# Optimization experiments

Hardware: AMD Instinct MI355X
Metric: run time of the kernel (lower is better)

## Reference

```python
import jax, jax.numpy as jnp
import numpy as np

B, N, H = 128, 1024, 128          # graphs, nodes per graph, hidden size
K1, K2, K3 = 512, 256, 128        # ceil(ratio^l * N), ratio = 0.5
DEG = 8                           # avg degree
E = B * N * DEG                   # total edges (fixed, masked after pooling)


def gcn_conv(x, row, col, mask, W, b, n):
    h = x @ W
    deg = jax.ops.segment_sum(mask, col, num_segments=n) + 1.0  # + self loop
    dinv = jax.lax.rsqrt(deg)
    coef = (dinv[row] * dinv[col] * mask)[:, None]
    agg = jax.ops.segment_sum(h[row] * coef, col, num_segments=n)
    return agg + h * (dinv * dinv)[:, None] + b  # self-loop term + bias


def topk_pool(x, row, col, mask, p, n_graphs, n_per, k):
    # PyG TopKPooling: y = x.p/||p||, keep per-graph top-k, x' = x[perm]*tanh(y[perm])
    score = (x @ p) / jnp.linalg.norm(p)
    vals, idx = jax.lax.top_k(score.reshape(n_graphs, n_per), k)  # [B, k]
    sel = (idx + (jnp.arange(n_graphs) * n_per)[:, None]).reshape(-1)
    xs = x[sel] * jnp.tanh(vals.reshape(-1))[:, None]
    # relabel edges; drop edges touching removed nodes via mask
    newid = jnp.full((n_graphs * n_per,), -1, jnp.int32).at[sel].set(
        jnp.arange(n_graphs * k, dtype=jnp.int32))
    nr, nc = newid[row], newid[col]
    nmask = mask * ((nr >= 0) & (nc >= 0)).astype(mask.dtype)
    return xs, jnp.maximum(nr, 0), jnp.maximum(nc, 0), nmask


def readout(x, n_graphs, k):
    # cat([gmp, gap]) with contiguous equal-size graphs
    xg = x.reshape(n_graphs, k, -1)
    return jnp.concatenate([xg.max(axis=1), xg.mean(axis=1)], axis=1)


def _forward(x, edge_row, edge_col, W1, b1, p1, W2, b2, p2, W3, b3, p3):
    mask = jnp.ones((E,), x.dtype)
    h = jax.nn.relu(gcn_conv(x, edge_row, edge_col, mask, W1, b1, B * N))
    x1, r, c, m = topk_pool(h, edge_row, edge_col, mask, p1, B, N, K1)
    out = readout(x1, B, K1)
    h = jax.nn.relu(gcn_conv(x1, r, c, m, W2, b2, B * K1))
    x2, r, c, m = topk_pool(h, r, c, m, p2, B, K1, K2)
    out = out + readout(x2, B, K2)
    h = jax.nn.relu(gcn_conv(x2, r, c, m, W3, b3, B * K2))
    x3, r, c, m = topk_pool(h, r, c, m, p3, B, K2, K3)
    out = out + readout(x3, B, K3)
    return out  # [B, 2*H]


def setup_inputs() -> dict:
    key = jax.random.key(0)
    ks = jax.random.split(key, 12)
    x = jax.random.normal(ks[0], (B * N, H), jnp.float32)
    off = (jnp.arange(B, dtype=jnp.int32) * N)[:, None]
    edge_row = (jax.random.randint(ks[1], (B, N * DEG), 0, N, jnp.int32) + off).reshape(-1)
    edge_col = (jax.random.randint(ks[2], (B, N * DEG), 0, N, jnp.int32) + off).reshape(-1)
    s = 1.0 / np.sqrt(H)
    params = {}
    for i, tag in enumerate(["1", "2", "3"]):
        params["W" + tag] = jax.random.normal(ks[3 + 3 * i], (H, H), jnp.float32) * s
        params["b" + tag] = jnp.zeros((H,), jnp.float32)
        params["p" + tag] = jax.random.normal(ks[4 + 3 * i], (H,), jnp.float32)
    return {"x": x, "edge_row": edge_row, "edge_col": edge_col, **params}


def reference(x, edge_row, edge_col, W1, b1, p1, W2, b2, p2, W3, b3, p3):
    return _forward(x, edge_row, edge_col, W1, b1, p1, W2, b2, p2, W3, b3, p3)
```

## Files before the change

kernel.cpp:

```cpp
#include <hip/hip_runtime.h>
#include <math.h>

#define BG   128
#define NPER 1024
#define HDIM 128
#define NEDGE (BG * NPER * 8)
#define NMAX (BG * NPER)
#define EPG  (NEDGE / BG)
#define CAP  48
#define PRE  16

typedef __attribute__((ext_vector_type(8))) short s16x8;
typedef __attribute__((ext_vector_type(4))) float f32x4;

static __device__ __forceinline__ ushort f2bf(float f) {
  uint u = __float_as_uint(f);
  return (ushort)((u + 0x7fffu + ((u >> 16) & 1u)) >> 16);
}
static __device__ __forceinline__ float bf2f(ushort h) {
  return __uint_as_float(((uint)h) << 16);
}

extern __shared__ float ldsbuf[];


__global__ __launch_bounds__(1024) void countfill_lds_kernel(
    const int* __restrict__ cr, const int* __restrict__ cc,
    int* __restrict__ cnt, int* __restrict__ meta8,
    int* __restrict__ srcext, int* __restrict__ order,
    int* __restrict__ odeg) {
  int* smeta = (int*)ldsbuf;
  int* scnt  = smeta + NPER * PRE;
  int* sbb   = scnt + NPER;
  int g = blockIdx.x, t = threadIdx.x;
  scnt[t] = 0;
  if (t < 2) sbb[t] = 0;
  __syncthreads();

  const int4* cr4 = (const int4*)(cr + (size_t)g * EPG);
  const int4* cc4 = (const int4*)(cc + (size_t)g * EPG);
  #pragma unroll
  for (int i = 0; i < 2; ++i) {
    int4 r = cr4[t * 2 + i];
    int4 c = cc4[t * 2 + i];
    int rl, cl, pos;
    cl = c.x & (NPER - 1); rl = r.x & (NPER - 1);
    pos = atomicAdd(&scnt[cl], 1);
    if (pos < PRE) smeta[cl * PRE + pos] = rl;
    else if (pos < CAP) srcext[((size_t)g * NPER + cl) * CAP + pos] = rl;
    cl = c.y & (NPER - 1); rl = r.y & (NPER - 1);
    pos = atomicAdd(&scnt[cl], 1);
    if (pos < PRE) smeta[cl * PRE + pos] = rl;
    else if (pos < CAP) srcext[((size_t)g * NPER + cl) * CAP + pos] = rl;
    cl = c.z & (NPER - 1); rl = r.z & (NPER - 1);
    pos = atomicAdd(&scnt[cl], 1);
    if (pos < PRE) smeta[cl * PRE + pos] = rl;
    else if (pos < CAP) srcext[((size_t)g * NPER + cl) * CAP + pos] = rl;
    cl = c.w & (NPER - 1); rl = r.w & (NPER - 1);
    pos = atomicAdd(&scnt[cl], 1);
    if (pos < PRE) smeta[cl * PRE + pos] = rl;
    else if (pos < CAP) srcext[((size_t)g * NPER + cl) * CAP + pos] = rl;
  }
  __syncthreads();

  int4* mo = (int4*)(meta8 + (size_t)g * NPER * PRE);
  const int4* sm4 = (const int4*)smeta;
  #pragma unroll
  for (int i = 0; i < 4; ++i) mo[i * 1024 + t] = sm4[i * 1024 + t];
  int d = scnt[t];
  cnt[g * NPER + t] = d;

  int bkt = d > 8 ? 1 : 0;
  int bpos = atomicAdd(&sbb[bkt], 1);
  __syncthreads();
  int slot = bkt ? sbb[0] + bpos : bpos;
  order[g * NPER + slot] = t;
  odeg[g * NPER + slot] = d;
}


__global__ __launch_bounds__(1024) void agg_lds_kernel(
    const float* __restrict__ x, float* __restrict__ z,
    const int* __restrict__ meta8, const int* __restrict__ srcext,
    const int* __restrict__ deg, const int* __restrict__ order,
    const int* __restrict__ odeg, int npg) {
  float* sX = ldsbuf;
  float* sDinv = sX + npg * 32;
  int g = blockIdx.x >> 2;
  int chunk = blockIdx.x & 3;
  int t = threadIdx.x;
  int base = g * npg;

  const float4* x4 = (const float4*)x;
  float4* sX4 = (float4*)sX;
  for (int i = t; i < npg * 8; i += 1024) {
    int r = i >> 3, l8 = i & 7;
    float dv = rsqrtf((float)deg[base + r] + 1.0f);
    float4 v = x4[(size_t)(base + r) * 32 + chunk * 8 + l8];
    v.x *= dv; v.y *= dv; v.z *= dv; v.w *= dv;
    sX4[i] = v;
  }
  for (int i = t; i < npg; i += 1024)
    sDinv[i] = rsqrtf((float)deg[base + i] + 1.0f);

  int dl = t >> 3, l = t & 7;
  const int4* m4 = (const int4*)meta8;
  float4* z4 = (float4*)z;

  int ordc = order[base + dl];
  int dpc  = odeg[base + dl];
  int ordn = order[base + dl + 128];
  int dpn  = odeg[base + dl + 128];
  int4 c0 = m4[(size_t)(base + ordc) * 4 + 0];
  int4 c1 = m4[(size_t)(base + ordc) * 4 + 1];
  int4 c2 = {0, 0, 0, 0}, c3 = {0, 0, 0, 0};
  if (dpc > 8) {
    c2 = m4[(size_t)(base + ordc) * 4 + 2];
    c3 = m4[(size_t)(base + ordc) * 4 + 3];
  }

  __syncthreads();

  for (int slot = dl; slot < npg; slot += 128) {
    int ordn2 = ordn, dpn2 = dpn;
    if (slot + 256 < npg) {
      ordn2 = order[base + slot + 256];
      dpn2  = odeg[base + slot + 256];
    }
    int4 n0 = {0,0,0,0}, n1 = {0,0,0,0}, n2 = {0,0,0,0}, n3 = {0,0,0,0};
    if (slot + 128 < npg) {
      n0 = m4[(size_t)(base + ordn) * 4 + 0];
      n1 = m4[(size_t)(base + ordn) * 4 + 1];
      if (dpn > 8) {
        n2 = m4[(size_t)(base + ordn) * 4 + 2];
        n3 = m4[(size_t)(base + ordn) * 4 + 3];
      }
    }

    int dst = ordc;
    int node = base + dst;
    int d = dpc > CAP ? CAP : dpc;
    int dp = d > PRE ? PRE : d;
    float dc = sDinv[dst];

    int sA0 = (0 < dp) ? c0.x : dst;
    int sA1 = (1 < dp) ? c0.y : dst;
    int sA2 = (2 < dp) ? c0.z : dst;
    int sA3 = (3 < dp) ? c0.w : dst;
    int sA4 = (4 < dp) ? c1.x : dst;
    int sA5 = (5 < dp) ? c1.y : dst;
    int sA6 = (6 < dp) ? c1.z : dst;
    int sA7 = (7 < dp) ? c1.w : dst;
    float4 w  = sX4[dst * 8 + l];
    float4 p0 = sX4[sA0 * 8 + l];
    float4 p1 = sX4[sA1 * 8 + l];
    float4 p2 = sX4[sA2 * 8 + l];
    float4 p3 = sX4[sA3 * 8 + l];
    float4 p4 = sX4[sA4 * 8 + l];
    float4 p5 = sX4[sA5 * 8 + l];
    float4 p6 = sX4[sA6 * 8 + l];
    float4 p7 = sX4[sA7 * 8 + l];
    float4 a0, a1, a2, a3;
    a0.x = w.x + p0.x; a0.y = w.y + p0.y; a0.z = w.z + p0.z; a0.w = w.w + p0.w;
    a1.x = p1.x + p5.x; a1.y = p1.y + p5.y; a1.z = p1.z + p5.z; a1.w = p1.w + p5.w;
    a2.x = p2.x + p6.x; a2.y = p2.y + p6.y; a2.z = p2.z + p6.z; a2.w = p2.w + p6.w;
    a3.x = p3.x + p7.x; a3.y = p3.y + p7.y; a3.z = p3.z + p7.z; a3.w = p3.w + p7.w;
    a0.x += p4.x; a0.y += p4.y; a0.z += p4.z; a0.w += p4.w;

    int nslots = 8;
    if (dp > 8) {
      int sB0 = (8 < dp)  ? c2.x : dst;
      int sB1 = (9 < dp)  ? c2.y : dst;
      int sB2 = (10 < dp) ? c2.z : dst;
      int sB3 = (11 < dp) ? c2.w : dst;
      int sB4 = (12 < dp) ? c3.x : dst;
      int sB5 = (13 < dp) ? c3.y : dst;
      int sB6 = (14 < dp) ? c3.z : dst;
      int sB7 = (15 < dp) ? c3.w : dst;
      float4 q0 = sX4[sB0 * 8 + l];
      float4 q1 = sX4[sB1 * 8 + l];
      float4 q2 = sX4[sB2 * 8 + l];
      float4 q3 = sX4[sB3 * 8 + l];
      float4 q4 = sX4[sB4 * 8 + l];
      float4 q5 = sX4[sB5 * 8 + l];
      float4 q6 = sX4[sB6 * 8 + l];
      float4 q7 = sX4[sB7 * 8 + l];
      a0.x += q0.x; a0.y += q0.y; a0.z += q0.z; a0.w += q0.w;
      a1.x += q1.x; a1.y += q1.y; a1.z += q1.z; a1.w += q1.w;
      a2.x += q2.x; a2.y += q2.y; a2.z += q2.z; a2.w += q2.w;
      a3.x += q3.x; a3.y += q3.y; a3.z += q3.z; a3.w += q3.w;
      a0.x += q4.x; a0.y += q4.y; a0.z += q4.z; a0.w += q4.w;
      a1.x += q5.x; a1.y += q5.y; a1.z += q5.z; a1.w += q5.w;
      a2.x += q6.x; a2.y += q6.y; a2.z += q6.z; a2.w += q6.w;
      a3.x += q7.x; a3.y += q7.y; a3.z += q7.z; a3.w += q7.w;
      nslots = 16;
    }

    if (d > PRE) {
      for (int e2 = PRE; e2 < d; ++e2) {
        int rl = srcext[(size_t)node * CAP + e2];
        float4 v0 = sX4[rl * 8 + l];
        a0.x += v0.x; a0.y += v0.y; a0.z += v0.z; a0.w += v0.w;
      }
    }

    float corr = (float)(nslots - dp);
    float4 o;
    o.x = (a0.x + a1.x + a2.x + a3.x - corr * w.x) * dc;
    o.y = (a0.y + a1.y + a2.y + a3.y - corr * w.y) * dc;
    o.z = (a0.z + a1.z + a2.z + a3.z - corr * w.z) * dc;
    o.w = (a0.w + a1.w + a2.w + a3.w - corr * w.w) * dc;
    z4[(size_t)node * 32 + chunk * 8 + l] = o;

    ordc = ordn; dpc = dpn; ordn = ordn2; dpn = dpn2;
    c0 = n0; c1 = n1; c2 = n2; c3 = n3;
  }
}


__global__ __launch_bounds__(256) void wsplit_kernel(
    const float* __restrict__ W0, const float* __restrict__ W1,
    const float* __restrict__ W2, ushort* __restrict__ wpk) {
  int id = blockIdx.x * 256 + threadIdx.x;
  int L = id >> 14;
  int r = id & 16383;
  int i = r & 7;
  int lane = (r >> 3) & 63;
  int nt = (r >> 9) & 7;
  int kt = (r >> 12) & 3;
  int k = kt * 32 + (lane >> 4) * 8 + i;
  int n = nt * 16 + (lane & 15);
  const float* W = (L == 0) ? W0 : (L == 1) ? W1 : W2;
  float v = W[k * HDIM + n];
  ushort h = f2bf(v);
  float r1 = v - bf2f(h);
  ushort m = f2bf(r1);
  ushort lo = f2bf(r1 - bf2f(m));
  size_t base = (size_t)L * 3 * 16384 + (size_t)r;
  wpk[base] = h;
  wpk[base + 16384] = m;
  wpk[base + 32768] = lo;
}


__global__ __launch_bounds__(256) void conv_mfma_kernel(
    float* __restrict__ zh, const ushort* __restrict__ wpk,
    const float* __restrict__ bias, const float* __restrict__ p,
    float* __restrict__ score) {
  __shared__ short sB[2][12288];
  int t = threadIdx.x;
  int wv = t >> 6, l = t & 63;
  int lr = l & 15, lq = l >> 4;
  int arowA = blockIdx.x * 128 + wv * 16 + lr;
  int arowB = arowA + 64;
  const float* zrowA = zh + (size_t)arowA * HDIM + lq * 8;
  const float* zrowB = zh + (size_t)arowB * HDIM + lq * 8;

  const int4* wp4 = (const int4*)wpk;
  int i0 = t, i1 = t + 256, i2 = t + 512;
  int i3 = t + 768, i4 = t + 1024, i5 = t + 1280;
  int s0 = (i0 >> 9) * 2048 + (i0 & 511);
  int s1 = (i1 >> 9) * 2048 + (i1 & 511);
  int s2 = (i2 >> 9) * 2048 + (i2 & 511);
  int s3 = (i3 >> 9) * 2048 + (i3 & 511);
  int s4 = (i4 >> 9) * 2048 + (i4 & 511);
  int s5 = (i5 >> 9) * 2048 + (i5 & 511);

  int4 rg0 = wp4[s0], rg1 = wp4[s1], rg2 = wp4[s2];
  int4 rg3 = wp4[s3], rg4 = wp4[s4], rg5 = wp4[s5];
  float4 cA0 = ((const float4*)zrowA)[0];
  float4 cA1 = ((const float4*)zrowA)[1];
  float4 cB0 = ((const float4*)zrowB)[0];
  float4 cB1 = ((const float4*)zrowB)[1];
  {
    int4* sw = (int4*)sB[0];
    sw[i0] = rg0; sw[i1] = rg1; sw[i2] = rg2;
    sw[i3] = rg3; sw[i4] = rg4; sw[i5] = rg5;
  }
  __syncthreads();

  f32x4 accA[8], accB[8];
  #pragma unroll
  for (int nt = 0; nt < 8; ++nt) { accA[nt] = (f32x4)(0.f); accB[nt] = (f32x4)(0.f); }

  for (int kt = 0; kt < 4; ++kt) {
    int cur = kt & 1;
    float4 nA0, nA1, nB0, nB1;
    if (kt < 3) {
      int kb = (kt + 1) * 512;
      rg0 = wp4[s0 + kb]; rg1 = wp4[s1 + kb]; rg2 = wp4[s2 + kb];
      rg3 = wp4[s3 + kb]; rg4 = wp4[s4 + kb]; rg5 = wp4[s5 + kb];
      nA0 = ((const float4*)(zrowA + (kt + 1) * 32))[0];
      nA1 = ((const float4*)(zrowA + (kt + 1) * 32))[1];
      nB0 = ((const float4*)(zrowB + (kt + 1) * 32))[0];
      nB1 = ((const float4*)(zrowB + (kt + 1) * 32))[1];
    }

    s16x8 ahA, amA, alA, ahB, amB, alB;
    float fA[8] = {cA0.x, cA0.y, cA0.z, cA0.w, cA1.x, cA1.y, cA1.z, cA1.w};
    float fB[8] = {cB0.x, cB0.y, cB0.z, cB0.w, cB1.x, cB1.y, cB1.z, cB1.w};
    #pragma unroll
    for (int i = 0; i < 8; ++i) {
      ushort h = f2bf(fA[i]);
      float r1 = fA[i] - bf2f(h);
      ushort m = f2bf(r1);
      ushort lo = f2bf(r1 - bf2f(m));
      ahA[i] = (short)h; amA[i] = (short)m; alA[i] = (short)lo;
      h = f2bf(fB[i]);
      r1 = fB[i] - bf2f(h);
      m = f2bf(r1);
      lo = f2bf(r1 - bf2f(m));
      ahB[i] = (short)h; amB[i] = (short)m; alB[i] = (short)lo;
    }

    const s16x8* sb = (const s16x8*)sB[cur];
    #pragma unroll
    for (int nt = 0; nt < 8; ++nt) {
      s16x8 bh = sb[nt * 64 + l];
      s16x8 bm = sb[512 + nt * 64 + l];
      s16x8 bl = sb[1024 + nt * 64 + l];
      accA[nt] = __builtin_amdgcn_mfma_f32_16x16x32_bf16(ahA, bh, accA[nt], 0, 0, 0);
      accA[nt] = __builtin_amdgcn_mfma_f32_16x16x32_bf16(ahA, bm, accA[nt], 0, 0, 0);
      accA[nt] = __builtin_amdgcn_mfma_f32_16x16x32_bf16(amA, bh, accA[nt], 0, 0, 0);
      accA[nt] = __builtin_amdgcn_mfma_f32_16x16x32_bf16(ahA, bl, accA[nt], 0, 0, 0);
      accA[nt] = __builtin_amdgcn_mfma_f32_16x16x32_bf16(alA, bh, accA[nt], 0, 0, 0);
      accA[nt] = __builtin_amdgcn_mfma_f32_16x16x32_bf16(amA, bm, accA[nt], 0, 0, 0);
      accB[nt] = __builtin_amdgcn_mfma_f32_16x16x32_bf16(ahB, bh, accB[nt], 0, 0, 0);
      accB[nt] = __builtin_amdgcn_mfma_f32_16x16x32_bf16(ahB, bm, accB[nt], 0, 0, 0);
      accB[nt] = __builtin_amdgcn_mfma_f32_16x16x32_bf16(amB, bh, accB[nt], 0, 0, 0);
      accB[nt] = __builtin_amdgcn_mfma_f32_16x16x32_bf16(ahB, bl, accB[nt], 0, 0, 0);
      accB[nt] = __builtin_amdgcn_mfma_f32_16x16x32_bf16(alB, bh, accB[nt], 0, 0, 0);
      accB[nt] = __builtin_amdgcn_mfma_f32_16x16x32_bf16(amB, bm, accB[nt], 0, 0, 0);
    }
    __syncthreads();
    if (kt < 3) {
      int4* sw = (int4*)sB[cur ^ 1];
      sw[i0] = rg0; sw[i1] = rg1; sw[i2] = rg2;
      sw[i3] = rg3; sw[i4] = rg4; sw[i5] = rg5;
      cA0 = nA0; cA1 = nA1; cB0 = nB0; cB1 = nB1;
    }
    __syncthreads();
  }

  int orowA = blockIdx.x * 128 + wv * 16 + lq * 4;
  int orowB = orowA + 64;
  float partA[4] = {0.f, 0.f, 0.f, 0.f};
  float partB[4] = {0.f, 0.f, 0.f, 0.f};
  #pragma unroll
  for (int nt = 0; nt < 8; ++nt) {
    float bv = bias[nt * 16 + lr];
    float pv = p[nt * 16 + lr];
    #pragma unroll
    for (int j = 0; j < 4; ++j) {
      float hA = fmaxf(accA[nt][j] + bv, 0.f);
      partA[j] += hA * pv;
      zh[(size_t)(orowA + j) * HDIM + nt * 16 + lr] = hA;
      float hB = fmaxf(accB[nt][j] + bv, 0.f);
      partB[j] += hB * pv;
      zh[(size_t)(orowB + j) * HDIM + nt * 16 + lr] = hB;
    }
  }
  #pragma unroll
  for (int j = 0; j < 4; ++j) {
    #pragma unroll
    for (int s = 1; s < 16; s <<= 1) {
      partA[j] += __shfl_xor(partA[j], s);
      partB[j] += __shfl_xor(partB[j], s);
    }
    if (lr == 0) {
      score[orowA + j] = partA[j];
      score[orowB + j] = partB[j];
    }
  }
}


__global__ __launch_bounds__(1024) void topk_mega_kernel(
    const float* __restrict__ score, const float* __restrict__ p,
    const float* __restrict__ h, float* __restrict__ xo,
    const int* __restrict__ in_r, const int* __restrict__ in_c,
    int* __restrict__ out_r, int* __restrict__ out_c,
    int* __restrict__ meta8, int* __restrict__ srcext,
    int* __restrict__ cnt, float* __restrict__ acc,
    int* __restrict__ order, int* __restrict__ odeg,
    float* __restrict__ outf, int P, int K, int L) {
  __shared__ float sv[1024];
  __shared__ int si[1024];
  __shared__ int snew[1024];
  __shared__ int scnt[512];
  __shared__ int bb[2];
  __shared__ float s_pn;
  __shared__ float4 smx[32][32], ssm[32][32];
  int g = blockIdx.x;
  int t = threadIdx.x;

  if (L < 2 && t < 512) scnt[t] = 0;
  if (t < 2) bb[t] = 0;
  snew[t] = -1;
  if (t < 128) { float v = p[t]; sv[t] = v * v; }
  __syncthreads();
  for (int off = 64; off; off >>= 1) {
    if (t < off) sv[t] += sv[t + off];
    __syncthreads();
  }
  if (t == 0) s_pn = sqrtf(sv[0]);
  __syncthreads();
  float pn = s_pn;

  sv[t] = score[(size_t)g * P + t];
  si[t] = t;
  for (int size = 2; size <= P; size <<= 1) {
    for (int stride = size >> 1; stride; stride >>= 1) {
      __syncthreads();
      int j = t ^ stride;
      if (j > t) {
        float a = sv[t], b = sv[j];
        int ia = si[t], ib = si[j];
        bool tFirst = (a > b) || (a == b && ia < ib);
        bool up = ((t & size) == 0);
        if (up ? !tFirst : tFirst) {
          sv[t] = b; sv[j] = a;
          si[t] = ib; si[j] = ia;
        }
      }
    }
  }
  __syncthreads();
  if (t < K) {
    snew[si[t]] = t;
    sv[t] = tanhf(sv[t] / pn);
  }
  __syncthreads();

  int lane = t & 31, grp = t >> 5;
  const float4* h4 = (const float4*)h;
  float4* xo4 = (float4*)xo;
  size_t hbase = (size_t)g * P * 32;
  float4 mx = make_float4(-INFINITY, -INFINITY, -INFINITY, -INFINITY);
  float4 sm = make_float4(0.f, 0.f, 0.f, 0.f);
  #pragma unroll
  for (int i = 0; i < 16; ++i) {
    int j = grp * 16 + i;
    float th = sv[j];
    float4 v = h4[hbase + (size_t)si[j] * 32 + lane];
    v.x *= th; v.y *= th; v.z *= th; v.w *= th;
    xo4[((size_t)g * K + j) * 32 + lane] = v;
    mx.x = fmaxf(mx.x, v.x); mx.y = fmaxf(mx.y, v.y);
    mx.z = fmaxf(mx.z, v.z); mx.w = fmaxf(mx.w, v.w);
    sm.x += v.x; sm.y += v.y; sm.z += v.z; sm.w += v.w;
  }
  smx[grp][lane] = mx;
  ssm[grp][lane] = sm;
  __syncthreads();
  int ngrp = P >> 5;
  if (grp == 0) {
    for (int s2 = 1; s2 < ngrp; ++s2) {
      float4 m2 = smx[s2][lane], s3 = ssm[s2][lane];
      mx.x = fmaxf(mx.x, m2.x); mx.y = fmaxf(mx.y, m2.y);
      mx.z = fmaxf(mx.z, m2.z); mx.w = fmaxf(mx.w, m2.w);
      sm.x += s3.x; sm.y += s3.y; sm.z += s3.z; sm.w += s3.w;
    }
    int c0 = lane * 4;
    if (L < 2) {
      float* amax = acc + (size_t)L * BG * 256 + (size_t)g * 256;
      float* asum = amax + 128;
      amax[c0 + 0] = mx.x; amax[c0 + 1] = mx.y;
      amax[c0 + 2] = mx.z; amax[c0 + 3] = mx.w;
      asum[c0 + 0] = sm.x; asum[c0 + 1] = sm.y;
      asum[c0 + 2] = sm.z; asum[c0 + 3] = sm.w;
    } else {
      sv[c0 + 0] = mx.x; sv[c0 + 1] = mx.y;
      sv[c0 + 2] = mx.z; sv[c0 + 3] = mx.w;
      sv[128 + c0 + 0] = sm.x; sv[128 + c0 + 1] = sm.y;
      sv[128 + c0 + 2] = sm.z; sv[128 + c0 + 3] = sm.w;
    }
  }

  if (L == 2) {
    __syncthreads();
    float v;
    const float* a0 = acc + (size_t)g * 256;
    const float* a1 = acc + (size_t)BG * 256 + (size_t)g * 256;
    if (t < 128) {
      v = a0[t] + a1[t] + sv[t];
    } else {
      v = a0[t] * (1.f / 512.f) + a1[t] * (1.f / 256.f) + sv[t] * (1.f / 128.f);
    }
    outf[g * 256 + t] = v;
    return;
  }

  int ept = EPG / P;
  int ebase = g * EPG;
  for (int i = 0; i < ept; ++i) {
    int e = ebase + i * P + t;
    int r = in_r[e];
    int nr = -1, nc = -1;
    if (r >= 0) {
      nr = snew[r & (P - 1)];
      nc = snew[in_c[e] & (P - 1)];
    }
    bool ok = (nr >= 0) && (nc >= 0);
    out_r[e] = ok ? g * K + nr : -1;
    out_c[e] = ok ? g * K + nc : -1;
    if (ok) {
      int pos = atomicAdd(&scnt[nc], 1);
      size_t gnode = (size_t)g * K + nc;
      if (pos < PRE) {
        meta8[gnode * PRE + pos] = nr;
      } else if (pos < CAP) {
        srcext[gnode * CAP + pos] = nr;
      }
    }
  }
  __syncthreads();
  if (t < K) cnt[g * K + t] = scnt[t];

  int bkt = 0, bpos = 0, bdeg = 0;
  if (t < K) {
    bdeg = scnt[t];
    bkt = bdeg > 8 ? 1 : 0;
    bpos = atomicAdd(&bb[bkt], 1);
  }
  __syncthreads();
  if (t < K) {
    int slot = bkt ? bb[0] + bpos : bpos;
    order[g * K + slot] = t;
    odeg[g * K + slot] = bdeg;
  }
}


extern "C" void kernel_launch(void* const* d_in, const int* in_sizes, int n_in,
                              void* d_out, int out_size, void* d_ws, size_t ws_size,
                              hipStream_t stream) {
  const float* x0 = (const float*)d_in[0];
  const int* erow = (const int*)d_in[1];
  const int* ecol = (const int*)d_in[2];
  const float* Wm[3] = {(const float*)d_in[3], (const float*)d_in[6], (const float*)d_in[9]};
  const float* bm[3] = {(const float*)d_in[4], (const float*)d_in[7], (const float*)d_in[10]};
  const float* pm[3] = {(const float*)d_in[5], (const float*)d_in[8], (const float*)d_in[11]};

  char* w = (char*)d_ws;
  size_t off = 0;
  auto alloc = [&](size_t bytes) -> void* {
    void* ptr = w + off;
    off = (off + bytes + 255) & ~(size_t)255;
    return ptr;
  };
  int* cur_row = (int*)alloc((size_t)NEDGE * 4);
  int* cur_col = (int*)alloc((size_t)NEDGE * 4);
  int* meta8   = (int*)alloc((size_t)NMAX * PRE * 4);
  int* srcext  = (int*)alloc((size_t)NMAX * CAP * 4);
  int* cnt     = (int*)alloc((size_t)NMAX * 4);
  int* order   = (int*)alloc((size_t)NMAX * 4);
  int* odeg    = (int*)alloc((size_t)NMAX * 4);
  float* score = (float*)alloc((size_t)NMAX * 4);
  float* acc   = (float*)alloc((size_t)2 * BG * 256 * 4);
  float* zh    = (float*)alloc((size_t)NMAX * HDIM * 4);
  float* x1    = (float*)alloc((size_t)BG * 512 * HDIM * 4);
  float* x2    = (float*)alloc((size_t)BG * 256 * HDIM * 4);
  float* x3    = (float*)alloc((size_t)BG * 128 * HDIM * 4);
  ushort* wpk  = (ushort*)alloc((size_t)3 * 3 * 16384 * 2);

  hipFuncSetAttribute((const void*)agg_lds_kernel,
                      hipFuncAttributeMaxDynamicSharedMemorySize, 152 * 1024);
  hipFuncSetAttribute((const void*)countfill_lds_kernel,
                      hipFuncAttributeMaxDynamicSharedMemorySize, 72 * 1024);

  size_t cfLds = (size_t)(NPER * PRE + NPER + 2) * 4;
  countfill_lds_kernel<<<BG, 1024, cfLds, stream>>>(
      erow, ecol, cnt, meta8, srcext, order, odeg);
  wsplit_kernel<<<(3 * 16384) / 256, 256, 0, stream>>>(Wm[0], Wm[1], Wm[2], wpk);

  const float* xin = x0;
  float* xout[3] = {x1, x2, x3};
  int Ps[3] = {1024, 512, 256};

  for (int L = 0; L < 3; ++L) {
    int P = Ps[L];
    int K = P >> 1;
    int n = BG * P;
    const int* in_r = (L == 0) ? erow : cur_row;
    const int* in_c = (L == 0) ? ecol : cur_col;
    size_t ldsBytes = (size_t)(P * 33) * 4;

    agg_lds_kernel<<<BG * 4, 1024, ldsBytes, stream>>>(
        xin, zh, meta8, srcext, cnt, order, odeg, P);
    conv_mfma_kernel<<<n / 128, 256, 0, stream>>>(
        zh, wpk + (size_t)L * 3 * 16384, bm[L], pm[L], score);
    topk_mega_kernel<<<BG, P, 0, stream>>>(
        score, pm[L], zh, xout[L], in_r, in_c, cur_row, cur_col,
        meta8, srcext, cnt, acc, order, odeg, (float*)d_out, P, K, L);
    xin = xout[L];
  }
}
```

Baseline: 317.6 us.

## Pack neighbor lists as 16-bit indices and transpose LDS feature layout

Stores the first 16 neighbor source indices per node as ushort rather than int, halving the meta array and its global loads and LDS footprint in countfill. The agg kernel's LDS feature tile is also transposed to a lane-major layout with a padded stride (npg+2), which is meant to change the LDS bank-conflict pattern of the gathered float4 reads. This adds unpacking shifts and masks per neighbor, and relies on local node ids fitting in 16 bits.

Result: no change. 316.1 us (-0.5%).

```diff
diff --git a/kernel.cpp b/kernel.cpp
--- a/kernel.cpp
+++ b/kernel.cpp
@@ -26,11 +26,11 @@
 
 __global__ __launch_bounds__(1024) void countfill_lds_kernel(
     const int* __restrict__ cr, const int* __restrict__ cc,
-    int* __restrict__ cnt, int* __restrict__ meta8,
+    int* __restrict__ cnt, ushort* __restrict__ meta16,
     int* __restrict__ srcext, int* __restrict__ order,
     int* __restrict__ odeg) {
-  int* smeta = (int*)ldsbuf;
-  int* scnt  = smeta + NPER * PRE;
+  ushort* smeta = (ushort*)ldsbuf;
+  int* scnt  = (int*)(smeta + NPER * PRE);
   int* sbb   = scnt + NPER;
   int g = blockIdx.x, t = threadIdx.x;
   scnt[t] = 0;
@@ -46,27 +46,27 @@
     int rl, cl, pos;
     cl = c.x & (NPER - 1); rl = r.x & (NPER - 1);
     pos = atomicAdd(&scnt[cl], 1);
-    if (pos < PRE) smeta[cl * PRE + pos] = rl;
+    if (pos < PRE) smeta[cl * PRE + pos] = (ushort)rl;
     else if (pos < CAP) srcext[((size_t)g * NPER + cl) * CAP + pos] = rl;
     cl = c.y & (NPER - 1); rl = r.y & (NPER - 1);
     pos = atomicAdd(&scnt[cl], 1);
-    if (pos < PRE) smeta[cl * PRE + pos] = rl;
+    if (pos < PRE) smeta[cl * PRE + pos] = (ushort)rl;
     else if (pos < CAP) srcext[((size_t)g * NPER + cl) * CAP + pos] = rl;
     cl = c.z & (NPER - 1); rl = r.z & (NPER - 1);
     pos = atomicAdd(&scnt[cl], 1);
-    if (pos < PRE) smeta[cl * PRE + pos] = rl;
+    if (pos < PRE) smeta[cl * PRE + pos] = (ushort)rl;
     else if (pos < CAP) srcext[((size_t)g * NPER + cl) * CAP + pos] = rl;
     cl = c.w & (NPER - 1); rl = r.w & (NPER - 1);
     pos = atomicAdd(&scnt[cl], 1);
-    if (pos < PRE) smeta[cl * PRE + pos] = rl;
+    if (pos < PRE) smeta[cl * PRE + pos] = (ushort)rl;
     else if (pos < CAP) srcext[((size_t)g * NPER + cl) * CAP + pos] = rl;
   }
   __syncthreads();
 
-  int4* mo = (int4*)(meta8 + (size_t)g * NPER * PRE);
+  int4* mo = (int4*)(meta16 + (size_t)g * NPER * PRE);
   const int4* sm4 = (const int4*)smeta;
   #pragma unroll
-  for (int i = 0; i < 4; ++i) mo[i * 1024 + t] = sm4[i * 1024 + t];
+  for (int i = 0; i < 2; ++i) mo[i * 1024 + t] = sm4[i * 1024 + t];
   int d = scnt[t];
   cnt[g * NPER + t] = d;
 
@@ -81,43 +81,39 @@
 
 __global__ __launch_bounds__(1024) void agg_lds_kernel(
     const float* __restrict__ x, float* __restrict__ z,
-    const int* __restrict__ meta8, const int* __restrict__ srcext,
+    const ushort* __restrict__ meta16, const int* __restrict__ srcext,
     const int* __restrict__ deg, const int* __restrict__ order,
     const int* __restrict__ odeg, int npg) {
-  float* sX = ldsbuf;
-  float* sDinv = sX + npg * 32;
+  const int PSTR = npg + 2;
+  float4* sX4 = (float4*)ldsbuf;
+  float* sDinv = ldsbuf + 8 * PSTR * 4;
   int g = blockIdx.x >> 2;
   int chunk = blockIdx.x & 3;
   int t = threadIdx.x;
   int base = g * npg;
 
   const float4* x4 = (const float4*)x;
-  float4* sX4 = (float4*)sX;
   for (int i = t; i < npg * 8; i += 1024) {
     int r = i >> 3, l8 = i & 7;
     float dv = rsqrtf((float)deg[base + r] + 1.0f);
     float4 v = x4[(size_t)(base + r) * 32 + chunk * 8 + l8];
     v.x *= dv; v.y *= dv; v.z *= dv; v.w *= dv;
-    sX4[i] = v;
+    sX4[l8 * PSTR + r] = v;
   }
   for (int i = t; i < npg; i += 1024)
     sDinv[i] = rsqrtf((float)deg[base + i] + 1.0f);
 
   int dl = t >> 3, l = t & 7;
-  const int4* m4 = (const int4*)meta8;
+  const int4* m4 = (const int4*)meta16;
   float4* z4 = (float4*)z;
 
   int ordc = order[base + dl];
   int dpc  = odeg[base + dl];
   int ordn = order[base + dl + 128];
   int dpn  = odeg[base + dl + 128];
-  int4 c0 = m4[(size_t)(base + ordc) * 4 + 0];
-  int4 c1 = m4[(size_t)(base + ordc) * 4 + 1];
-  int4 c2 = {0, 0, 0, 0}, c3 = {0, 0, 0, 0};
-  if (dpc > 8) {
-    c2 = m4[(size_t)(base + ordc) * 4 + 2];
-    c3 = m4[(size_t)(base + ordc) * 4 + 3];
-  }
+  int4 c0 = m4[(size_t)(base + ordc) * 2 + 0];
+  int4 c1 = {0, 0, 0, 0};
+  if (dpc > 8) c1 = m4[(size_t)(base + ordc) * 2 + 1];
 
   __syncthreads();
 
@@ -127,14 +123,10 @@
       ordn2 = order[base + slot + 256];
       dpn2  = odeg[base + slot + 256];
     }
-    int4 n0 = {0,0,0,0}, n1 = {0,0,0,0}, n2 = {0,0,0,0}, n3 = {0,0,0,0};
+    int4 n0 = {0,0,0,0}, n1 = {0,0,0,0};
     if (slot + 128 < npg) {
-      n0 = m4[(size_t)(base + ordn) * 4 + 0];
-      n1 = m4[(size_t)(base + ordn) * 4 + 1];
-      if (dpn > 8) {
-        n2 = m4[(size_t)(base + ordn) * 4 + 2];
-        n3 = m4[(size_t)(base + ordn) * 4 + 3];
-      }
+      n0 = m4[(size_t)(base + ordn) * 2 + 0];
+      if (dpn > 8) n1 = m4[(size_t)(base + ordn) * 2 + 1];
     }
 
     int dst = ordc;
@@ -143,23 +135,29 @@
     int dp = d > PRE ? PRE : d;
     float dc = sDinv[dst];
 
-    int sA0 = (0 < dp) ? c0.x : dst;
-    int sA1 = (1 < dp) ? c0.y : dst;
-    int sA2 = (2 < dp) ? c0.z : dst;
-    int sA3 = (3 < dp) ? c0.w : dst;
-    int sA4 = (4 < dp) ? c1.x : dst;
-    int sA5 = (5 < dp) ? c1.y : dst;
-    int sA6 = (6 < dp) ? c1.z : dst;
-    int sA7 = (7 < dp) ? c1.w : dst;
-    float4 w  = sX4[dst * 8 + l];
-    float4 p0 = sX4[sA0 * 8 + l];
-    float4 p1 = sX4[sA1 * 8 + l];
-    float4 p2 = sX4[sA2 * 8 + l];
-    float4 p3 = sX4[sA3 * 8 + l];
-    float4 p4 = sX4[sA4 * 8 + l];
-    float4 p5 = sX4[sA5 * 8 + l];
-    float4 p6 = sX4[sA6 * 8 + l];
-    float4 p7 = sX4[sA7 * 8 + l];
+    int e0 = c0.x & 0xffff, e1 = ((uint)c0.x) >> 16;
+    int e2 = c0.y & 0xffff, e3 = ((uint)c0.y) >> 16;
+    int e4 = c0.z & 0xffff, e5 = ((uint)c0.z) >> 16;
+    int e6 = c0.w & 0xffff, e7 = ((uint)c0.w) >> 16;
+
+    int sA0 = (0 < dp) ? e0 : dst;
+    int sA1 = (1 < dp) ? e1 : dst;
+    int sA2 = (2 < dp) ? e2 : dst;
+    int sA3 = (3 < dp) ? e3 : dst;
+    int sA4 = (4 < dp) ? e4 : dst;
+    int sA5 = (5 < dp) ? e5 : dst;
+    int sA6 = (6 < dp) ? e6 : dst;
+    int sA7 = (7 < dp) ? e7 : dst;
+    int pb = l * PSTR;
+    float4 w  = sX4[pb + dst];
+    float4 p0 = sX4[pb + sA0];
+    float4 p1 = sX4[pb + sA1];
+    float4 p2 = sX4[pb + sA2];
+    float4 p3 = sX4[pb + sA3];
+    float4 p4 = sX4[pb + sA4];
+    float4 p5 = sX4[pb + sA5];
+    float4 p6 = sX4[pb + sA6];
+    float4 p7 = sX4[pb + sA7];
     float4 a0, a1, a2, a3;
     a0.x = w.x + p0.x; a0.y = w.y + p0.y; a0.z = w.z + p0.z; a0.w = w.w + p0.w;
     a1.x = p1.x + p5.x; a1.y = p1.y + p5.y; a1.z = p1.z + p5.z; a1.w = p1.w + p5.w;
@@ -169,22 +167,26 @@
 
     int nslots = 8;
     if (dp > 8) {
-      int sB0 = (8 < dp)  ? c2.x : dst;
-      int sB1 = (9 < dp)  ? c2.y : dst;
-      int sB2 = (10 < dp) ? c2.z : dst;
-      int sB3 = (11 < dp) ? c2.w : dst;
-      int sB4 = (12 < dp) ? c3.x : dst;
-      int sB5 = (13 < dp) ? c3.y : dst;
-      int sB6 = (14 < dp) ? c3.z : dst;
-      int sB7 = (15 < dp) ? c3.w : dst;
-      float4 q0 = sX4[sB0 * 8 + l];
-      float4 q1 = sX4[sB1 * 8 + l];
-      float4 q2 = sX4[sB2 * 8 + l];
-      float4 q3 = sX4[sB3 * 8 + l];
-      float4 q4 = sX4[sB4 * 8 + l];
-      float4 q5 = sX4[sB5 * 8 + l];
-      float4 q6 = sX4[sB6 * 8 + l];
-      float4 q7 = sX4[sB7 * 8 + l];
+      int f0 = c1.x & 0xffff, f1 = ((uint)c1.x) >> 16;
+      int f2 = c1.y & 0xffff, f3 = ((uint)c1.y) >> 16;
+      int f4 = c1.z & 0xffff, f5 = ((uint)c1.z) >> 16;
+      int f6 = c1.w & 0xffff, f7 = ((uint)c1.w) >> 16;
+      int sB0 = (8 < dp)  ? f0 : dst;
+      int sB1 = (9 < dp)  ? f1 : dst;
+      int sB2 = (10 < dp) ? f2 : dst;
+      int sB3 = (11 < dp) ? f3 : dst;
+      int sB4 = (12 < dp) ? f4 : dst;
+      int sB5 = (13 < dp) ? f5 : dst;
+      int sB6 = (14 < dp) ? f6 : dst;
+      int sB7 = (15 < dp) ? f7 : dst;
+      float4 q0 = sX4[pb + sB0];
+      float4 q1 = sX4[pb + sB1];
+      float4 q2 = sX4[pb + sB2];
+      float4 q3 = sX4[pb + sB3];
+      float4 q4 = sX4[pb + sB4];
+      float4 q5 = sX4[pb + sB5];
+      float4 q6 = sX4[pb + sB6];
+      float4 q7 = sX4[pb + sB7];
       a0.x += q0.x; a0.y += q0.y; a0.z += q0.z; a0.w += q0.w;
       a1.x += q1.x; a1.y += q1.y; a1.z += q1.z; a1.w += q1.w;
       a2.x += q2.x; a2.y += q2.y; a2.z += q2.z; a2.w += q2.w;
@@ -197,9 +199,9 @@
     }
 
     if (d > PRE) {
-      for (int e2 = PRE; e2 < d; ++e2) {
-        int rl = srcext[(size_t)node * CAP + e2];
-        float4 v0 = sX4[rl * 8 + l];
+      for (int e2i = PRE; e2i < d; ++e2i) {
+        int rl = srcext[(size_t)node * CAP + e2i];
+        float4 v0 = sX4[pb + rl];
         a0.x += v0.x; a0.y += v0.y; a0.z += v0.z; a0.w += v0.w;
       }
     }
@@ -213,7 +215,7 @@
     z4[(size_t)node * 32 + chunk * 8 + l] = o;
 
     ordc = ordn; dpc = dpn; ordn = ordn2; dpn = dpn2;
-    c0 = n0; c1 = n1; c2 = n2; c3 = n3;
+    c0 = n0; c1 = n1;
   }
 }
 
@@ -380,7 +382,7 @@
     const float* __restrict__ h, float* __restrict__ xo,
     const int* __restrict__ in_r, const int* __restrict__ in_c,
     int* __restrict__ out_r, int* __restrict__ out_c,
-    int* __restrict__ meta8, int* __restrict__ srcext,
+    ushort* __restrict__ meta16, int* __restrict__ srcext,
     int* __restrict__ cnt, float* __restrict__ acc,
     int* __restrict__ order, int* __restrict__ odeg,
     float* __restrict__ outf, int P, int K, int L) {
@@ -507,7 +509,7 @@
       int pos = atomicAdd(&scnt[nc], 1);
       size_t gnode = (size_t)g * K + nc;
       if (pos < PRE) {
-        meta8[gnode * PRE + pos] = nr;
+        meta16[gnode * PRE + pos] = (ushort)nr;
       } else if (pos < CAP) {
         srcext[gnode * CAP + pos] = nr;
       }
@@ -550,7 +552,7 @@
   };
   int* cur_row = (int*)alloc((size_t)NEDGE * 4);
   int* cur_col = (int*)alloc((size_t)NEDGE * 4);
-  int* meta8   = (int*)alloc((size_t)NMAX * PRE * 4);
+  ushort* meta16 = (ushort*)alloc((size_t)NMAX * PRE * 2);
   int* srcext  = (int*)alloc((size_t)NMAX * CAP * 4);
   int* cnt     = (int*)alloc((size_t)NMAX * 4);
   int* order   = (int*)alloc((size_t)NMAX * 4);
@@ -565,12 +567,10 @@
 
   hipFuncSetAttribute((const void*)agg_lds_kernel,
                       hipFuncAttributeMaxDynamicSharedMemorySize, 152 * 1024);
-  hipFuncSetAttribute((const void*)countfill_lds_kernel,
-                      hipFuncAttributeMaxDynamicSharedMemorySize, 72 * 1024);
-
-  size_t cfLds = (size_t)(NPER * PRE + NPER + 2) * 4;
+
+  size_t cfLds = (size_t)(NPER * PRE * 2 + NPER * 4 + 8);
   countfill_lds_kernel<<<BG, 1024, cfLds, stream>>>(
-      erow, ecol, cnt, meta8, srcext, order, odeg);
+      erow, ecol, cnt, meta16, srcext, order, odeg);
   wsplit_kernel<<<(3 * 16384) / 256, 256, 0, stream>>>(Wm[0], Wm[1], Wm[2], wpk);
 
   const float* xin = x0;
@@ -583,15 +583,15 @@
     int n = BG * P;
     const int* in_r = (L == 0) ? erow : cur_row;
     const int* in_c = (L == 0) ? ecol : cur_col;
-    size_t ldsBytes = (size_t)(P * 33) * 4;
+    size_t ldsBytes = (size_t)(8 * (P + 2) * 16 + P * 4);
 
     agg_lds_kernel<<<BG * 4, 1024, ldsBytes, stream>>>(
-        xin, zh, meta8, srcext, cnt, order, odeg, P);
+        xin, zh, meta16, srcext, cnt, order, odeg, P);
     conv_mfma_kernel<<<n / 128, 256, 0, stream>>>(
         zh, wpk + (size_t)L * 3 * 16384, bm[L], pm[L], score);
     topk_mega_kernel<<<BG, P, 0, stream>>>(
         score, pm[L], zh, xout[L], in_r, in_c, cur_row, cur_col,
-        meta8, srcext, cnt, acc, order, odeg, (float*)d_out, P, K, L);
+        meta16, srcext, cnt, acc, order, odeg, (float*)d_out, P, K, L);
     xin = xout[L];
   }
 }
```
